# Optimization experiments

Hardware: AMD Instinct MI355X
Metric: run time of the kernel (lower is better)

The kernel has to match this reference:

```python
import jax, jax.numpy as jnp
import numpy as np

N_NODES = 50000
N_EDGES = 800000
F_IN = 512
HID = 128
OUT = 20


def setup_inputs() -> dict:
    key = jax.random.key(0)
    k1, k2, k3, k4, k5 = jax.random.split(key, 5)
    x = jax.random.normal(k1, (N_NODES, F_IN), dtype=jnp.float32)
    edge_index = jax.random.randint(k2, (2, N_EDGES), 0, N_NODES, dtype=jnp.int64)
    edge_weight = jax.random.uniform(k3, (N_EDGES,), dtype=jnp.float32)
    W1 = jax.random.normal(k4, (F_IN, HID), dtype=jnp.float32) * 0.05
    b1 = jnp.zeros((HID,), dtype=jnp.float32)
    W2 = jax.random.normal(k5, (HID, OUT), dtype=jnp.float32) * 0.05
    b2 = jnp.zeros((OUT,), dtype=jnp.float32)
    return {"x": x, "edge_index": edge_index, "edge_weight": edge_weight,
            "W1": W1, "b1": b1, "W2": W2, "b2": b2}


def _gcn_norm(edge_index, edge_weight, num_nodes):
    # PyG gcn_norm: add self-loops (weight 1), symmetric D^-1/2 (A+I) D^-1/2
    row, col = edge_index[0], edge_index[1]
    loop = jnp.arange(num_nodes, dtype=row.dtype)
    row = jnp.concatenate([row, loop])
    col = jnp.concatenate([col, loop])
    w = jnp.concatenate([edge_weight, jnp.ones((num_nodes,), edge_weight.dtype)])
    deg = jax.ops.segment_sum(w, col, num_segments=num_nodes)
    dinv = jnp.where(deg > 0, jax.lax.rsqrt(deg), 0.0)
    norm = dinv[row] * w * dinv[col]
    return row, col, norm


def _gcn_conv(x, W, b, row, col, norm, num_nodes):
    # linear first (in >= out), then gather-scale-scatter aggregation
    h = x @ W                              # [N, out]
    msg = h[row] * norm[:, None]           # [E+N, out]
    out = jax.ops.segment_sum(msg, col, num_segments=num_nodes)
    return out + b


def reference(x, edge_index, edge_weight, W1, b1, W2, b2):
    n = x.shape[0]
    row, col, norm = _gcn_norm(edge_index, edge_weight, n)
    h = jax.nn.relu(_gcn_conv(x, W1, b1, row, col, norm, n))
    # dropout p=0.6 is identity in eval mode
    out = _gcn_conv(h, W2, b2, row, col, norm, n)
    return out
```

## Files before the change

### kernel.cpp

```cpp
#include <hip/hip_runtime.h>

#define N_NODES 50000
#define N_EDGES 800000
#define F_IN    512
#define HID     128
#define OUT_F   20
#define CAP     48

#define BM  32
#define GEMM_BLOCKS ((N_NODES + BM - 1) / BM)
#define FB_BLOCKS   521
#define FAT_BLOCKS  (FB_BLOCKS * 4)

typedef __bf16 bf16x8 __attribute__((ext_vector_type(8)));
typedef float  f32x4  __attribute__((ext_vector_type(4)));


__global__ void k_prep(const float* __restrict__ W1, __bf16* __restrict__ w1p,
                       int* __restrict__ cursor) {
    int gidx = blockIdx.x * blockDim.x + threadIdx.x;
    if (gidx < F_IN * HID) {
        int k  = gidx >> 7;
        int cc = gidx & (HID - 1);
        int kk = k >> 5;
        int r  = k & 31;
        int g  = (r & 15) >> 2;
        int j  = (r & 3) + ((r >> 4) << 2);
        w1p[((((size_t)kk * 4 + g) * 128 + cc) << 3) + j] = (__bf16)W1[gidx];
    }
    if (gidx < N_NODES) cursor[gidx] = gidx * CAP;
}


__global__ __launch_bounds__(256) void k_fat(const float* __restrict__ x,
                                             const __bf16* __restrict__ w1p,
                                             __bf16* __restrict__ hb,
                                             const int* __restrict__ row,
                                             const int* __restrict__ col,
                                             const float* __restrict__ ew,
                                             int* __restrict__ cursor,
                                             uint2* __restrict__ packed) {
    __shared__ float As[2][BM * 64];
    const int tid = threadIdx.x;
    const int q   = blockIdx.x >> 2;
    const int r3  = blockIdx.x & 3;

    if (r3 == 3) {
        for (int v = q * 256 + tid; v < N_EDGES / 4; v += FB_BLOCKS * 256) {
            int4   c4 = ((const int4*)col)[v];
            int4   r4 = ((const int4*)row)[v];
            float4 w4 = ((const float4*)ew)[v];
            int p0 = atomicAdd(&cursor[c4.x], 1);
            int p1 = atomicAdd(&cursor[c4.y], 1);
            int p2 = atomicAdd(&cursor[c4.z], 1);
            int p3 = atomicAdd(&cursor[c4.w], 1);
            packed[p0] = make_uint2((unsigned)r4.x, __float_as_uint(w4.x));
            packed[p1] = make_uint2((unsigned)r4.y, __float_as_uint(w4.y));
            packed[p2] = make_uint2((unsigned)r4.z, __float_as_uint(w4.z));
            packed[p3] = make_uint2((unsigned)r4.w, __float_as_uint(w4.w));
        }
        return;
    }

    const int gemm_id = q * 3 + r3;
    const int lane = tid & 63;
    const int wid  = tid >> 6;
    const int wm   = wid >> 1;
    const int wn   = wid & 1;
    const int r0   = gemm_id * BM;
    const int g    = lane >> 4;
    const int l15  = lane & 15;

    const __bf16* pb = w1p + (((size_t)g * 128) + wn * 64 + l15) * 8;

    f32x4 acc0 = {}, acc1 = {}, acc2 = {}, acc3 = {};

    auto stage = [&](int buf, int k0) {
#pragma unroll
        for (int i = 0; i < 2; ++i) {
            int cb = wid * 64 + i * 256;
            int c  = cb + lane;
            int rowc = c >> 4;
            int s    = c & 15;
            int gr = r0 + rowc;
            if (gr >= N_NODES) gr = N_NODES - 1;
            const float* src = x + (size_t)gr * F_IN + k0 + ((s ^ (rowc & 7)) << 2);
            __builtin_amdgcn_global_load_lds(
                (const __attribute__((address_space(1))) void*)src,
                (__attribute__((address_space(3))) void*)(&As[buf][(size_t)cb * 4]),
                16, 0, 0);
        }
    };

    const int rowm = wm * 16 + l15;
    const int rbase = rowm * 64;
    const int rx = rowm & 7;

    stage(0, 0);
    __syncthreads();

#pragma unroll
    for (int t = 0; t < 8; ++t) {
        const int buf = t & 1;
        if (t < 7) stage(buf ^ 1, (t + 1) * 64);
#pragma unroll
        for (int kk = 0; kk < 2; ++kk) {
            int slo = ((kk * 8 + g)     ^ rx) << 2;
            int shi = ((kk * 8 + g + 4) ^ rx) << 2;
            f32x4 lo = *(const f32x4*)&As[buf][rbase + slo];
            f32x4 hi = *(const f32x4*)&As[buf][rbase + shi];
            union { __bf16 h[8]; bf16x8 v; } u;
            u.h[0] = (__bf16)lo[0]; u.h[1] = (__bf16)lo[1];
            u.h[2] = (__bf16)lo[2]; u.h[3] = (__bf16)lo[3];
            u.h[4] = (__bf16)hi[0]; u.h[5] = (__bf16)hi[1];
            u.h[6] = (__bf16)hi[2]; u.h[7] = (__bf16)hi[3];
            const __bf16* bp = pb + (size_t)(t * 2 + kk) * 4096;
            bf16x8 b0 = *(const bf16x8*)(bp);
            bf16x8 b1 = *(const bf16x8*)(bp + 128);
            bf16x8 b2 = *(const bf16x8*)(bp + 256);
            bf16x8 b3 = *(const bf16x8*)(bp + 384);
            acc0 = __builtin_amdgcn_mfma_f32_16x16x32_bf16(u.v, b0, acc0, 0, 0, 0);
            acc1 = __builtin_amdgcn_mfma_f32_16x16x32_bf16(u.v, b1, acc1, 0, 0, 0);
            acc2 = __builtin_amdgcn_mfma_f32_16x16x32_bf16(u.v, b2, acc2, 0, 0, 0);
            acc3 = __builtin_amdgcn_mfma_f32_16x16x32_bf16(u.v, b3, acc3, 0, 0, 0);
        }
        __syncthreads();
    }

    const int rb = r0 + wm * 16 + (g << 2);
#pragma unroll
    for (int rr = 0; rr < 4; ++rr) {
        int gr = rb + rr;
        if (gr < N_NODES) {
            __bf16* ho = hb + (size_t)gr * HID + wn * 64 + l15;
            ho[0]  = (__bf16)acc0[rr];
            ho[16] = (__bf16)acc1[rr];
            ho[32] = (__bf16)acc2[rr];
            ho[48] = (__bf16)acc3[rr];
        }
    }
}


__global__ void k_degdinv(const int* __restrict__ cursor, const uint2* __restrict__ packed,
                          int* __restrict__ cnt, float* __restrict__ dinv) {
    int i = blockIdx.x * blockDim.x + threadIdx.x;
    if (i < N_NODES) {
        int n = cursor[i] - i * CAP;
        cnt[i] = n;
        const uint2* seg = packed + (size_t)i * CAP;
        float d = 1.0f;
        for (int k = 0; k < n; ++k) d += __uint_as_float(seg[k].y);
        dinv[i] = rsqrtf(d);
    }
}


__device__ inline float blo(unsigned v) { union { unsigned u; float f; } c; c.u = v << 16; return c.f; }
__device__ inline float bhi(unsigned v) { union { unsigned u; float f; } c; c.u = v & 0xffff0000u; return c.f; }

__global__ __launch_bounds__(128) void k_agg1g2(uint2* __restrict__ packed,
                                                const int* __restrict__ cnt,
                                                const __bf16* __restrict__ hb,
                                                const float* __restrict__ dinv,
                                                const float* __restrict__ b1,
                                                const float* __restrict__ W2,
                                                float* __restrict__ h2) {
    __shared__ int   sr[2][64];
    __shared__ float sn[2][64];
    __shared__ float sh1[2][128];
    const int w    = threadIdx.x >> 6;
    const int lane = threadIdx.x & 63;
    const int c    = blockIdx.x * 2 + w;
    const unsigned* hbu = (const unsigned*)hb;

    float dic = dinv[c];
    unsigned sv = hbu[((size_t)c << 6) + lane];
    float a0 = dic * dic * blo(sv);
    float a1 = dic * dic * bhi(sv);
    int n = cnt[c];
    uint2* seg = packed + (size_t)c * CAP;
    for (int base = 0; base < n; base += 64) {
        int m = n - base; if (m > 64) m = 64;
        if (lane < m) {
            uint2 pv = seg[base + lane];
            float nm = __uint_as_float(pv.y) * dinv[pv.x] * dic;
            sr[w][lane] = (int)pv.x;
            sn[w][lane] = nm;
            seg[base + lane] = make_uint2(pv.x, __float_as_uint(nm));
        }
        for (int t = 0; t < m; ++t) {
            float nm = sn[w][t];
            unsigned v = hbu[((size_t)sr[w][t] << 6) + lane];
            a0 = fmaf(nm, blo(v), a0);
            a1 = fmaf(nm, bhi(v), a1);
        }
    }
    float2 bb = *(const float2*)(b1 + 2 * lane);
    a0 += bb.x; a1 += bb.y;
    sh1[w][2 * lane]     = a0 > 0.f ? a0 : 0.f;
    sh1[w][2 * lane + 1] = a1 > 0.f ? a1 : 0.f;

    const int part = lane / 20;
    const int j    = lane - part * 20;
    float s = 0.f;
    if (part < 3) {
        const int kbeg = part * 43;
        const int kend = (part == 2) ? 128 : kbeg + 43;
#pragma unroll 4
        for (int k = kbeg; k < kend; ++k)
            s = fmaf(sh1[w][k], W2[k * OUT_F + j], s);
    }
    float s1 = __shfl(s, lane + 20);
    float s2 = __shfl(s, lane + 40);
    if (lane < 20) h2[(size_t)c * OUT_F + lane] = s + s1 + s2;
}


__global__ __launch_bounds__(256) void k_agg2(const uint2* __restrict__ packed,
                                              const int* __restrict__ cnt,
                                              const float* __restrict__ h2,
                                              const float* __restrict__ dinv,
                                              const float* __restrict__ b2,
                                              float* __restrict__ out) {
    int g = blockIdx.x * blockDim.x + threadIdx.x;
    int c = g >> 5;
    int j = g & 31;
    if (c >= N_NODES || j >= OUT_F) return;
    float dic = dinv[c];
    float acc = dic * dic * h2[(size_t)c * OUT_F + j] + b2[j];
    int n = cnt[c];
    const uint2* seg = packed + (size_t)c * CAP;
    for (int k = 0; k < n; ++k) {
        uint2 pv = seg[k];
        acc = fmaf(__uint_as_float(pv.y), h2[(size_t)pv.x * OUT_F + j], acc);
    }
    out[(size_t)c * OUT_F + j] = acc;
}


extern "C" void kernel_launch(void* const* d_in, const int* in_sizes, int n_in,
                              void* d_out, int out_size, void* d_ws, size_t ws_size,
                              hipStream_t stream) {
    const float* x  = (const float*)d_in[0];
    const int*   ei = (const int*)d_in[1];
    const float* ew = (const float*)d_in[2];
    const float* W1 = (const float*)d_in[3];
    const float* b1 = (const float*)d_in[4];
    const float* W2 = (const float*)d_in[5];
    const float* b2 = (const float*)d_in[6];
    float* out = (float*)d_out;

    const int* row = ei;
    const int* col = ei + N_EDGES;

    char* p = (char*)d_ws;
    float* dinv    = (float*)p;    p += (size_t)N_NODES * 4;
    float* h2      = (float*)p;    p += (size_t)N_NODES * OUT_F * 4;
    __bf16* hb     = (__bf16*)p;   p += (size_t)N_NODES * HID * 2;
    __bf16* w1p    = (__bf16*)p;   p += (size_t)F_IN * HID * 2;
    int* cursor    = (int*)p;      p += (size_t)N_NODES * 4;
    int* cnt       = (int*)p;      p += (size_t)N_NODES * 4;
    uint2* packed  = (uint2*)p;    p += (size_t)N_NODES * CAP * 8;

    k_prep<<<(F_IN * HID + 255) / 256, 256, 0, stream>>>(W1, w1p, cursor);

    k_fat<<<FAT_BLOCKS, 256, 0, stream>>>(x, w1p, hb, row, col, ew, cursor, packed);

    k_degdinv<<<(N_NODES + 255) / 256, 256, 0, stream>>>(cursor, packed, cnt, dinv);

    k_agg1g2<<<N_NODES / 2, 128, 0, stream>>>(packed, cnt, hb, dinv, b1, W2, h2);

    k_agg2<<<(N_NODES * 32 + 255) / 256, 256, 0, stream>>>(packed, cnt, h2, dinv, b2, out);
}
```

Before: 174.6 us.

## Stage W1 tiles in LDS with triple-buffered async pipeline over k=32 steps

The GEMM main loop now stages both the x tile and the packed bf16 W1 tile into LDS with async global_load_lds, using three buffers and 32-wide k steps. Explicit vmcnt waits keep two stages in flight, replacing the former double buffer where each wave read W1 fragments straight from global memory. This is meant to hide global load latency and cut repeated global reads of W1 across waves. In exchange it uses more LDS per block, which could lower occupancy, and it needs two barriers per k step.

```diff
diff --git a/kernel.cpp b/kernel.cpp
--- a/kernel.cpp
+++ b/kernel.cpp
@@ -40,7 +40,8 @@
                                              const float* __restrict__ ew,
                                              int* __restrict__ cursor,
                                              uint2* __restrict__ packed) {
-    __shared__ float As[2][BM * 64];
+    __shared__ float  As[3][BM * 32];
+    __shared__ __bf16 Bs[3][4096];
     const int tid = threadIdx.x;
     const int q   = blockIdx.x >> 2;
     const int r3  = blockIdx.x & 3;
@@ -71,60 +72,69 @@
     const int g    = lane >> 4;
     const int l15  = lane & 15;
 
-    const __bf16* pb = w1p + (((size_t)g * 128) + wn * 64 + l15) * 8;
-
     f32x4 acc0 = {}, acc1 = {}, acc2 = {}, acc3 = {};
 
-    auto stage = [&](int buf, int k0) {
+    auto stage = [&](int buf, int t) {
+        {
+            int c    = (wid << 6) + lane;
+            int rowc = c >> 3;
+            int s    = c & 7;
+            int gr   = r0 + rowc;
+            if (gr >= N_NODES) gr = N_NODES - 1;
+            const float* src = x + (size_t)gr * F_IN + (t << 5) + ((s ^ (rowc & 7)) << 2);
+            __builtin_amdgcn_global_load_lds(
+                (const __attribute__((address_space(1))) void*)src,
+                (__attribute__((address_space(3))) void*)(&As[buf][(size_t)c * 4]),
+                16, 0, 0);
+        }
 #pragma unroll
         for (int i = 0; i < 2; ++i) {
-            int cb = wid * 64 + i * 256;
-            int c  = cb + lane;
-            int rowc = c >> 4;
-            int s    = c & 15;
-            int gr = r0 + rowc;
-            if (gr >= N_NODES) gr = N_NODES - 1;
-            const float* src = x + (size_t)gr * F_IN + k0 + ((s ^ (rowc & 7)) << 2);
+            int c = (wid << 7) + (i << 6) + lane;
+            const __bf16* srcb = w1p + (size_t)t * 4096 + (size_t)c * 8;
             __builtin_amdgcn_global_load_lds(
-                (const __attribute__((address_space(1))) void*)src,
-                (__attribute__((address_space(3))) void*)(&As[buf][(size_t)cb * 4]),
+                (const __attribute__((address_space(1))) void*)srcb,
+                (__attribute__((address_space(3))) void*)(&Bs[buf][(size_t)c * 8]),
                 16, 0, 0);
         }
     };
 
-    const int rowm = wm * 16 + l15;
-    const int rbase = rowm * 64;
-    const int rx = rowm & 7;
+    const int rowm  = wm * 16 + l15;
+    const int rbase = rowm * 32;
+    const int rx    = rowm & 7;
+    const int bbase = (wn * 64 + l15) * 8;
 
     stage(0, 0);
-    __syncthreads();
+    stage(1, 1);
+    asm volatile("s_waitcnt vmcnt(3)" ::: "memory");
+    __builtin_amdgcn_s_barrier();
 
 #pragma unroll
-    for (int t = 0; t < 8; ++t) {
-        const int buf = t & 1;
-        if (t < 7) stage(buf ^ 1, (t + 1) * 64);
-#pragma unroll
-        for (int kk = 0; kk < 2; ++kk) {
-            int slo = ((kk * 8 + g)     ^ rx) << 2;
-            int shi = ((kk * 8 + g + 4) ^ rx) << 2;
-            f32x4 lo = *(const f32x4*)&As[buf][rbase + slo];
-            f32x4 hi = *(const f32x4*)&As[buf][rbase + shi];
-            union { __bf16 h[8]; bf16x8 v; } u;
-            u.h[0] = (__bf16)lo[0]; u.h[1] = (__bf16)lo[1];
-            u.h[2] = (__bf16)lo[2]; u.h[3] = (__bf16)lo[3];
-            u.h[4] = (__bf16)hi[0]; u.h[5] = (__bf16)hi[1];
-            u.h[6] = (__bf16)hi[2]; u.h[7] = (__bf16)hi[3];
-            const __bf16* bp = pb + (size_t)(t * 2 + kk) * 4096;
-            bf16x8 b0 = *(const bf16x8*)(bp);
-            bf16x8 b1 = *(const bf16x8*)(bp + 128);
-            bf16x8 b2 = *(const bf16x8*)(bp + 256);
-            bf16x8 b3 = *(const bf16x8*)(bp + 384);
-            acc0 = __builtin_amdgcn_mfma_f32_16x16x32_bf16(u.v, b0, acc0, 0, 0, 0);
-            acc1 = __builtin_amdgcn_mfma_f32_16x16x32_bf16(u.v, b1, acc1, 0, 0, 0);
-            acc2 = __builtin_amdgcn_mfma_f32_16x16x32_bf16(u.v, b2, acc2, 0, 0, 0);
-            acc3 = __builtin_amdgcn_mfma_f32_16x16x32_bf16(u.v, b3, acc3, 0, 0, 0);
-        }
-        __syncthreads();
+    for (int t = 0; t < 16; ++t) {
+        const int buf = t % 3;
+        if (t < 14) stage((t + 2) % 3, t + 2);
+        if (t < 14)      asm volatile("s_waitcnt vmcnt(6)" ::: "memory");
+        else if (t == 14) asm volatile("s_waitcnt vmcnt(3)" ::: "memory");
+        else              asm volatile("s_waitcnt vmcnt(0)" ::: "memory");
+        __builtin_amdgcn_s_barrier();
+
+        f32x4 lo = *(const f32x4*)&As[buf][rbase + ((g ^ rx) << 2)];
+        f32x4 hi = *(const f32x4*)&As[buf][rbase + (((g + 4) ^ rx) << 2)];
+        union { __bf16 h[8]; bf16x8 v; } u;
+        u.h[0] = (__bf16)lo[0]; u.h[1] = (__bf16)lo[1];
+        u.h[2] = (__bf16)lo[2]; u.h[3] = (__bf16)lo[3];
+        u.h[4] = (__bf16)hi[0]; u.h[5] = (__bf16)hi[1];
+        u.h[6] = (__bf16)hi[2]; u.h[7] = (__bf16)hi[3];
+        const __bf16* bp = &Bs[buf][g * 1024 + bbase];
+        bf16x8 b0 = *(const bf16x8*)(bp);
+        bf16x8 b1 = *(const bf16x8*)(bp + 128);
+        bf16x8 b2 = *(const bf16x8*)(bp + 256);
+        bf16x8 b3 = *(const bf16x8*)(bp + 384);
+        acc0 = __builtin_amdgcn_mfma_f32_16x16x32_bf16(u.v, b0, acc0, 0, 0, 0);
+        acc1 = __builtin_amdgcn_mfma_f32_16x16x32_bf16(u.v, b1, acc1, 0, 0, 0);
+        acc2 = __builtin_amdgcn_mfma_f32_16x16x32_bf16(u.v, b2, acc2, 0, 0, 0);
+        acc3 = __builtin_amdgcn_mfma_f32_16x16x32_bf16(u.v, b3, acc3, 0, 0, 0);
+
+        __builtin_amdgcn_s_barrier();
     }
 
     const int rb = r0 + wm * 16 + (g << 2);
```

Result: no change. 175.7 us (+0.6%).
